# Performance work log

Measured on AMD Instinct MI355X. Metric: run time of the kernel, lower is better.

Reference implementation:

```python
import jax, jax.numpy as jnp
import numpy as np
from jax import lax

B, T, I, H, O = 4096, 512, 10, 32, 1

def setup_inputs() -> dict:
    key = jax.random.key(0)
    ks = jax.random.split(key, 7)
    s = 1.0 / np.sqrt(H)
    return {
        "x": jax.random.normal(ks[0], (B, T, I), dtype=jnp.float32),
        "W_ih": jax.random.uniform(ks[1], (4 * H, I), minval=-s, maxval=s, dtype=jnp.float32),
        "W_hh": jax.random.uniform(ks[2], (4 * H, H), minval=-s, maxval=s, dtype=jnp.float32),
        "b_ih": jax.random.uniform(ks[3], (4 * H,), minval=-s, maxval=s, dtype=jnp.float32),
        "b_hh": jax.random.uniform(ks[4], (4 * H,), minval=-s, maxval=s, dtype=jnp.float32),
        "W_dense": jax.random.uniform(ks[5], (O, H), minval=-s, maxval=s, dtype=jnp.float32),
        "b_dense": jax.random.uniform(ks[6], (O,), minval=-s, maxval=s, dtype=jnp.float32),
    }

def reference(x, W_ih, W_hh, b_ih, b_hh, W_dense, b_dense):
    # x: [B, T, I]; PyTorch LSTM gate order: i, f, g, o.
    b, t, _ = x.shape
    h = W_hh.shape[1]
    # Precompute input contribution for all timesteps: [T, B, 4H]
    gates_x = jnp.einsum('bti,gi->tbg', x, W_ih) + b_ih + b_hh

    def step(carry, gx):
        h_prev, c_prev = carry
        g = gx + h_prev @ W_hh.T  # [B, 4H]
        i_g = jax.nn.sigmoid(g[:, 0 * h:1 * h])
        f_g = jax.nn.sigmoid(g[:, 1 * h:2 * h])
        g_g = jnp.tanh(g[:, 2 * h:3 * h])
        o_g = jax.nn.sigmoid(g[:, 3 * h:4 * h])
        c = f_g * c_prev + i_g * g_g
        h_new = o_g * jnp.tanh(c)
        return (h_new, c), None

    init = (jnp.zeros((b, h), x.dtype), jnp.zeros((b, h), x.dtype))
    (h_last, _), _ = lax.scan(step, init, gates_x)
    # dropout in eval mode = identity
    return h_last @ W_dense.T + b_dense
```

## Files before the change

kernel.cpp:

```cpp
#include <hip/hip_runtime.h>


#define T_SZ 512
#define I_SZ 10
#define H_SZ 32

typedef _Float16 half8  __attribute__((ext_vector_type(8)));
typedef __fp16   fp16x2 __attribute__((ext_vector_type(2)));
typedef float    f32x4  __attribute__((ext_vector_type(4)));
typedef int      i32x4  __attribute__((ext_vector_type(4)));

union FH { i32x4 i; half8 h; };
static __device__ __forceinline__ half8 fragv(i32x4 v) { FH u; u.i = v; return u.h; }
static __device__ __forceinline__ half8 frag4(int a, int b, int c, int d) {
    FH u; u.i = (i32x4){a, b, c, d}; return u.h;
}

static __device__ __forceinline__ int pk16(float lo, float hi) {
    union { fp16x2 h; int i; } u;
    u.h = __builtin_amdgcn_cvt_pkrtz(lo, hi);
    return u.i;
}

#define MFMAH(A, B, C) __builtin_amdgcn_mfma_f32_16x16x32_f16((A), (B), (C), 0, 0, 0)

__global__ __launch_bounds__(64, 2)
void lstm_wave(const float* __restrict__ x, const float* __restrict__ W_ih,
               const float* __restrict__ W_hh, const float* __restrict__ b_ih,
               const float* __restrict__ b_hh, const float* __restrict__ W_dense,
               const float* __restrict__ b_dense, float* __restrict__ out)
{
    const int lane  = threadIdx.x;
    const int L     = lane & 15;
    const int Q     = lane >> 4;
    const int bbase = blockIdx.x * 2;

    const int bA   = L >> 3;
    const int bAct = Q >> 1;
    const int hidA = L + 16 * (Q & 1);

    int bhh[8][4];
    int bm[8][4];
    #pragma unroll
    for (int tau = 0; tau < 8; ++tau) {
        const int wr = 32 * (tau >> 1) + 16 * (tau & 1) + L;
        const float* ph = W_hh + wr * H_SZ + 8 * Q;
        #pragma unroll
        for (int d = 0; d < 4; ++d) {
            float2 v = *(const float2*)(ph + 2 * d);
            bhh[tau][d] = pk16(v.x, v.y);
        }
        if (Q == 0) {
            const float* pi = W_ih + wr * I_SZ;
            #pragma unroll
            for (int d = 0; d < 4; ++d) {
                float2 v = *(const float2*)(pi + 2 * d);
                bm[tau][d] = pk16(v.x, v.y);
            }
        } else if (Q == 1) {
            float2 v = *(const float2*)(W_ih + wr * I_SZ + 8);
            bm[tau][0] = pk16(v.x, v.y);
            #pragma unroll
            for (int d = 1; d < 4; ++d) {
                float2 w = *(const float2*)(W_hh + wr * H_SZ + 8 + 2 * d);
                bm[tau][d] = pk16(w.x, w.y);
            }
        } else {
            bm[tau][0] = bhh[tau][0]; bm[tau][1] = bhh[tau][1];
            bm[tau][2] = bhh[tau][2]; bm[tau][3] = bhh[tau][3];
        }
    }

    const float nL = -1.4426950f;
    const float m2 = -2.8853901f;
    const float mbi = nL * (b_ih[hidA]          + b_hh[hidA]);
    const float mbf = nL * (b_ih[32 + hidA]     + b_hh[32 + hidA]);
    const float mbg = m2 * (b_ih[64 + hidA]     + b_hh[64 + hidA]);
    const float mbo = nL * (b_ih[96 + hidA]     + b_hh[96 + hidA]);

    __shared__ __attribute__((aligned(16))) _Float16 hbuf[2][2][2][H_SZ];
    {
        int* zz = (int*)&hbuf[0][0][0][0];
        zz[lane] = 0;
        zz[lane + 64] = 0;
    }

    const float* xrow = x + (size_t)(bbase + bA) * (T_SZ * I_SZ);
    float2 xa0 = *(const float2*)(xrow + 0), xa1 = *(const float2*)(xrow + 2),
           xa2 = *(const float2*)(xrow + 4), xa3 = *(const float2*)(xrow + 6),
           xa4 = *(const float2*)(xrow + 8);
    float2 xb0 = *(const float2*)(xrow + I_SZ + 0), xb1 = *(const float2*)(xrow + I_SZ + 2),
           xb2 = *(const float2*)(xrow + I_SZ + 4), xb3 = *(const float2*)(xrow + I_SZ + 6),
           xb4 = *(const float2*)(xrow + I_SZ + 8);

    const f32x4 zerov = {0.f, 0.f, 0.f, 0.f};
    float cst = 0.0f;
    float hlast = 0.0f;
    const bool q0 = (Q == 0), q1 = (Q == 1);

    for (int t = 0; t < T_SZ; t += 2) {
        #pragma unroll
        for (int u = 0; u < 2; ++u) {
            const int rb = u, wb = u ^ 1;

            const _Float16* hp = &hbuf[rb][0][bA][8 * Q];
            const _Float16* lp = &hbuf[rb][1][bA][8 * Q];
            i32x4 hhi_ = *(const i32x4*)hp;
            i32x4 lo_  = *(const i32x4*)lp;

            float2 y0 = u ? xb0 : xa0, y1 = u ? xb1 : xa1, y2 = u ? xb2 : xa2,
                   y3 = u ? xb3 : xa3, y4 = u ? xb4 : xa4;
            int p0 = pk16(y0.x, y0.y), p1 = pk16(y1.x, y1.y), p2 = pk16(y2.x, y2.y),
                p3 = pk16(y3.x, y3.y), p4 = pk16(y4.x, y4.y);

            half8 mf = fragv((i32x4){ q0 ? p0 : (q1 ? p4 : lo_[0]),
                                      q0 ? p1 : lo_[1],
                                      q0 ? p2 : lo_[2],
                                      q0 ? p3 : lo_[3] });

            if (t + 2 + u < T_SZ) {
                const float* xr = xrow + (t + 2 + u) * I_SZ;
                if (u == 0) {
                    xa0 = *(const float2*)(xr + 0); xa1 = *(const float2*)(xr + 2);
                    xa2 = *(const float2*)(xr + 4); xa3 = *(const float2*)(xr + 6);
                    xa4 = *(const float2*)(xr + 8);
                } else {
                    xb0 = *(const float2*)(xr + 0); xb1 = *(const float2*)(xr + 2);
                    xb2 = *(const float2*)(xr + 4); xb3 = *(const float2*)(xr + 6);
                    xb4 = *(const float2*)(xr + 8);
                }
            }

            half8 hhi = fragv(hhi_);
            float v[8];
            #pragma unroll
            for (int tau = 0; tau < 8; ++tau) {
                f32x4 acc = MFMAH(mf, frag4(bm[tau][0], bm[tau][1], bm[tau][2], bm[tau][3]), zerov);
                acc = MFMAH(hhi, frag4(bhh[tau][0], bhh[tau][1], bhh[tau][2], bhh[tau][3]), acc);
                v[tau] = acc[0];
            }

            const bool qh = (Q & 1);
            float vi = qh ? v[1] : v[0];
            float vf = qh ? v[3] : v[2];
            float vg = qh ? v[5] : v[4];
            float vo = qh ? v[7] : v[6];
            float ig = __builtin_amdgcn_rcpf(1.0f + __builtin_amdgcn_exp2f(fmaf(nL, vi, mbi)));
            float fg = __builtin_amdgcn_rcpf(1.0f + __builtin_amdgcn_exp2f(fmaf(nL, vf, mbf)));
            float gr = __builtin_amdgcn_rcpf(1.0f + __builtin_amdgcn_exp2f(fmaf(m2, vg, mbg)));
            float gg = fmaf(2.0f, gr, -1.0f);
            float og = __builtin_amdgcn_rcpf(1.0f + __builtin_amdgcn_exp2f(fmaf(nL, vo, mbo)));
            cst = fmaf(fg, cst, ig * gg);
            float tr = __builtin_amdgcn_rcpf(1.0f + __builtin_amdgcn_exp2f(m2 * cst));
            float th = fmaf(2.0f, tr, -1.0f);
            float h  = og * th;
            hlast = h;

            _Float16 hh = (_Float16)h;
            _Float16 hl = (_Float16)(h - (float)hh);
            hbuf[wb][0][bAct][hidA] = hh;
            hbuf[wb][1][bAct][hidA] = hl;
        }
    }

    float v = hlast * W_dense[hidA];
    #pragma unroll
    for (int m = 16; m >= 1; m >>= 1)
        v += __shfl_xor(v, m);
    if (lane == 0)  out[bbase + 0] = v + b_dense[0];
    if (lane == 32) out[bbase + 1] = v + b_dense[0];
}

extern "C" void kernel_launch(void* const* d_in, const int* in_sizes, int n_in,
                              void* d_out, int out_size, void* d_ws, size_t ws_size,
                              hipStream_t stream) {
    const float* x       = (const float*)d_in[0];
    const float* W_ih    = (const float*)d_in[1];
    const float* W_hh    = (const float*)d_in[2];
    const float* b_ih    = (const float*)d_in[3];
    const float* b_hh    = (const float*)d_in[4];
    const float* W_dense = (const float*)d_in[5];
    const float* b_dense = (const float*)d_in[6];
    float* out = (float*)d_out;

    lstm_wave<<<dim3(2048), dim3(64), 0, stream>>>(
        x, W_ih, W_hh, b_ih, b_hh, W_dense, b_dense, out);
}
```

Baseline: 363.4 us.

## Pack four batch rows per wave, halving grid and doubling per-lane gate work

Each 64-lane wave now handles four batch sequences instead of two. Every lane computes two hidden units, one from each half of the MFMA output, and the grid is halved. The intent is to use the otherwise redundant MFMA rows and cut wave count, trading fewer waves for a longer per-step serial activation chain in each lane. There is a risk of lower latency hiding, since each wave has a longer per-step critical path and fewer waves run overall.

```diff
diff --git a/kernel.cpp b/kernel.cpp
--- a/kernel.cpp
+++ b/kernel.cpp
@@ -24,7 +24,7 @@
 
 #define MFMAH(A, B, C) __builtin_amdgcn_mfma_f32_16x16x32_f16((A), (B), (C), 0, 0, 0)
 
-__global__ __launch_bounds__(64, 2)
+__global__ __launch_bounds__(64, 1)
 void lstm_wave(const float* __restrict__ x, const float* __restrict__ W_ih,
                const float* __restrict__ W_hh, const float* __restrict__ b_ih,
                const float* __restrict__ b_hh, const float* __restrict__ W_dense,
@@ -33,11 +33,10 @@
     const int lane  = threadIdx.x;
     const int L     = lane & 15;
     const int Q     = lane >> 4;
-    const int bbase = blockIdx.x * 2;
+    const int bbase = blockIdx.x * 4;
 
-    const int bA   = L >> 3;
-    const int bAct = Q >> 1;
-    const int hidA = L + 16 * (Q & 1);
+    const int bA = L >> 2;
+    const int h0 = L, h1 = L + 16;
 
     int bhh[8][4];
     int bm[8][4];
@@ -73,16 +72,19 @@
 
     const float nL = -1.4426950f;
     const float m2 = -2.8853901f;
-    const float mbi = nL * (b_ih[hidA]          + b_hh[hidA]);
-    const float mbf = nL * (b_ih[32 + hidA]     + b_hh[32 + hidA]);
-    const float mbg = m2 * (b_ih[64 + hidA]     + b_hh[64 + hidA]);
-    const float mbo = nL * (b_ih[96 + hidA]     + b_hh[96 + hidA]);
+    const float mbi0 = nL * (b_ih[h0]      + b_hh[h0]);
+    const float mbf0 = nL * (b_ih[32 + h0] + b_hh[32 + h0]);
+    const float mbg0 = m2 * (b_ih[64 + h0] + b_hh[64 + h0]);
+    const float mbo0 = nL * (b_ih[96 + h0] + b_hh[96 + h0]);
+    const float mbi1 = nL * (b_ih[h1]      + b_hh[h1]);
+    const float mbf1 = nL * (b_ih[32 + h1] + b_hh[32 + h1]);
+    const float mbg1 = m2 * (b_ih[64 + h1] + b_hh[64 + h1]);
+    const float mbo1 = nL * (b_ih[96 + h1] + b_hh[96 + h1]);
 
-    __shared__ __attribute__((aligned(16))) _Float16 hbuf[2][2][2][H_SZ];
+    __shared__ __attribute__((aligned(16))) _Float16 hbuf[2][2][4][H_SZ];
     {
         int* zz = (int*)&hbuf[0][0][0][0];
-        zz[lane] = 0;
-        zz[lane + 64] = 0;
+        zz[lane] = 0; zz[lane + 64] = 0; zz[lane + 128] = 0; zz[lane + 192] = 0;
     }
 
     const float* xrow = x + (size_t)(bbase + bA) * (T_SZ * I_SZ);
@@ -94,8 +96,8 @@
            xb4 = *(const float2*)(xrow + I_SZ + 8);
 
     const f32x4 zerov = {0.f, 0.f, 0.f, 0.f};
-    float cst = 0.0f;
-    float hlast = 0.0f;
+    float cst0 = 0.0f, cst1 = 0.0f;
+    float h0last = 0.0f, h1last = 0.0f;
     const bool q0 = (Q == 0), q1 = (Q == 1);
 
     for (int t = 0; t < T_SZ; t += 2) {
@@ -140,35 +142,44 @@
                 v[tau] = acc[0];
             }
 
-            const bool qh = (Q & 1);
-            float vi = qh ? v[1] : v[0];
-            float vf = qh ? v[3] : v[2];
-            float vg = qh ? v[5] : v[4];
-            float vo = qh ? v[7] : v[6];
-            float ig = __builtin_amdgcn_rcpf(1.0f + __builtin_amdgcn_exp2f(fmaf(nL, vi, mbi)));
-            float fg = __builtin_amdgcn_rcpf(1.0f + __builtin_amdgcn_exp2f(fmaf(nL, vf, mbf)));
-            float gr = __builtin_amdgcn_rcpf(1.0f + __builtin_amdgcn_exp2f(fmaf(m2, vg, mbg)));
-            float gg = fmaf(2.0f, gr, -1.0f);
-            float og = __builtin_amdgcn_rcpf(1.0f + __builtin_amdgcn_exp2f(fmaf(nL, vo, mbo)));
-            cst = fmaf(fg, cst, ig * gg);
-            float tr = __builtin_amdgcn_rcpf(1.0f + __builtin_amdgcn_exp2f(m2 * cst));
-            float th = fmaf(2.0f, tr, -1.0f);
-            float h  = og * th;
-            hlast = h;
+            float ig0 = __builtin_amdgcn_rcpf(1.0f + __builtin_amdgcn_exp2f(fmaf(nL, v[0], mbi0)));
+            float fg0 = __builtin_amdgcn_rcpf(1.0f + __builtin_amdgcn_exp2f(fmaf(nL, v[2], mbf0)));
+            float gr0 = __builtin_amdgcn_rcpf(1.0f + __builtin_amdgcn_exp2f(fmaf(m2, v[4], mbg0)));
+            float gg0 = fmaf(2.0f, gr0, -1.0f);
+            float og0 = __builtin_amdgcn_rcpf(1.0f + __builtin_amdgcn_exp2f(fmaf(nL, v[6], mbo0)));
+            cst0 = fmaf(fg0, cst0, ig0 * gg0);
+            float tr0 = __builtin_amdgcn_rcpf(1.0f + __builtin_amdgcn_exp2f(m2 * cst0));
+            float th0 = fmaf(2.0f, tr0, -1.0f);
+            float hv0 = og0 * th0;
+            h0last = hv0;
 
-            _Float16 hh = (_Float16)h;
-            _Float16 hl = (_Float16)(h - (float)hh);
-            hbuf[wb][0][bAct][hidA] = hh;
-            hbuf[wb][1][bAct][hidA] = hl;
+            float ig1 = __builtin_amdgcn_rcpf(1.0f + __builtin_amdgcn_exp2f(fmaf(nL, v[1], mbi1)));
+            float fg1 = __builtin_amdgcn_rcpf(1.0f + __builtin_amdgcn_exp2f(fmaf(nL, v[3], mbf1)));
+            float gr1 = __builtin_amdgcn_rcpf(1.0f + __builtin_amdgcn_exp2f(fmaf(m2, v[5], mbg1)));
+            float gg1 = fmaf(2.0f, gr1, -1.0f);
+            float og1 = __builtin_amdgcn_rcpf(1.0f + __builtin_amdgcn_exp2f(fmaf(nL, v[7], mbo1)));
+            cst1 = fmaf(fg1, cst1, ig1 * gg1);
+            float tr1 = __builtin_amdgcn_rcpf(1.0f + __builtin_amdgcn_exp2f(m2 * cst1));
+            float th1 = fmaf(2.0f, tr1, -1.0f);
+            float hv1 = og1 * th1;
+            h1last = hv1;
+
+            _Float16 a0h = (_Float16)hv0;
+            _Float16 a0l = (_Float16)(hv0 - (float)a0h);
+            _Float16 a1h = (_Float16)hv1;
+            _Float16 a1l = (_Float16)(hv1 - (float)a1h);
+            hbuf[wb][0][Q][h0] = a0h;
+            hbuf[wb][0][Q][h1] = a1h;
+            hbuf[wb][1][Q][h0] = a0l;
+            hbuf[wb][1][Q][h1] = a1l;
         }
     }
 
-    float v = hlast * W_dense[hidA];
+    float v = h0last * W_dense[h0] + h1last * W_dense[h1];
     #pragma unroll
-    for (int m = 16; m >= 1; m >>= 1)
+    for (int m = 8; m >= 1; m >>= 1)
         v += __shfl_xor(v, m);
-    if (lane == 0)  out[bbase + 0] = v + b_dense[0];
-    if (lane == 32) out[bbase + 1] = v + b_dense[0];
+    if (L == 0) out[bbase + Q] = v + b_dense[0];
 }
 
 extern "C" void kernel_launch(void* const* d_in, const int* in_sizes, int n_in,
@@ -183,6 +194,6 @@
     const float* b_dense = (const float*)d_in[6];
     float* out = (float*)d_out;
 
-    lstm_wave<<<dim3(2048), dim3(64), 0, stream>>>(
+    lstm_wave<<<dim3(1024), dim3(64), 0, stream>>>(
         x, W_ih, W_hh, b_ih, b_hh, W_dense, b_dense, out);
 }
```

After: 368.0 us. No clear change (+1.3%).

## Interleave two independent batch-pair recurrences per wave to hide MFMA latency

Applied to the files above, without the earlier changes.

Each 64-lane wave now advances two independent pairs of batch rows (four sequences) together, running the MFMA chains and gate math for both in the same timestep. The two dependency chains can overlap, filling MFMA and transcendental latency that a single serial recurrence leaves idle. The grid is halved to 1024 waves and launch bounds relaxed to one wave per EU, which raises register pressure and cuts the number of concurrent waves.

```diff
diff --git a/kernel.cpp b/kernel.cpp
--- a/kernel.cpp
+++ b/kernel.cpp
@@ -24,7 +24,7 @@
 
 #define MFMAH(A, B, C) __builtin_amdgcn_mfma_f32_16x16x32_f16((A), (B), (C), 0, 0, 0)
 
-__global__ __launch_bounds__(64, 2)
+__global__ __launch_bounds__(64, 1)
 void lstm_wave(const float* __restrict__ x, const float* __restrict__ W_ih,
                const float* __restrict__ W_hh, const float* __restrict__ b_ih,
                const float* __restrict__ b_hh, const float* __restrict__ W_dense,
@@ -33,9 +33,9 @@
     const int lane  = threadIdx.x;
     const int L     = lane & 15;
     const int Q     = lane >> 4;
-    const int bbase = blockIdx.x * 2;
-
-    const int bA   = L >> 3;
+    const int bbase = blockIdx.x * 4;
+
+    const int bAg  = L >> 3;
     const int bAct = Q >> 1;
     const int hidA = L + 16 * (Q & 1);
 
@@ -73,102 +73,154 @@
 
     const float nL = -1.4426950f;
     const float m2 = -2.8853901f;
-    const float mbi = nL * (b_ih[hidA]          + b_hh[hidA]);
-    const float mbf = nL * (b_ih[32 + hidA]     + b_hh[32 + hidA]);
-    const float mbg = m2 * (b_ih[64 + hidA]     + b_hh[64 + hidA]);
-    const float mbo = nL * (b_ih[96 + hidA]     + b_hh[96 + hidA]);
-
-    __shared__ __attribute__((aligned(16))) _Float16 hbuf[2][2][2][H_SZ];
+    const float mbi = nL * (b_ih[hidA]      + b_hh[hidA]);
+    const float mbf = nL * (b_ih[32 + hidA] + b_hh[32 + hidA]);
+    const float mbg = m2 * (b_ih[64 + hidA] + b_hh[64 + hidA]);
+    const float mbo = nL * (b_ih[96 + hidA] + b_hh[96 + hidA]);
+
+    __shared__ __attribute__((aligned(16))) _Float16 hbuf[2][2][4][H_SZ];
     {
         int* zz = (int*)&hbuf[0][0][0][0];
-        zz[lane] = 0;
-        zz[lane + 64] = 0;
-    }
-
-    const float* xrow = x + (size_t)(bbase + bA) * (T_SZ * I_SZ);
-    float2 xa0 = *(const float2*)(xrow + 0), xa1 = *(const float2*)(xrow + 2),
-           xa2 = *(const float2*)(xrow + 4), xa3 = *(const float2*)(xrow + 6),
-           xa4 = *(const float2*)(xrow + 8);
-    float2 xb0 = *(const float2*)(xrow + I_SZ + 0), xb1 = *(const float2*)(xrow + I_SZ + 2),
-           xb2 = *(const float2*)(xrow + I_SZ + 4), xb3 = *(const float2*)(xrow + I_SZ + 6),
-           xb4 = *(const float2*)(xrow + I_SZ + 8);
+        zz[lane] = 0; zz[lane + 64] = 0; zz[lane + 128] = 0; zz[lane + 192] = 0;
+    }
+
+    const float* xrowX = x + (size_t)(bbase + bAg)     * (T_SZ * I_SZ);
+    const float* xrowY = x + (size_t)(bbase + 2 + bAg) * (T_SZ * I_SZ);
+    float2 xA0 = *(const float2*)(xrowX + 0), xA1 = *(const float2*)(xrowX + 2),
+           xA2 = *(const float2*)(xrowX + 4), xA3 = *(const float2*)(xrowX + 6),
+           xA4 = *(const float2*)(xrowX + 8);
+    float2 xB0 = *(const float2*)(xrowX + I_SZ + 0), xB1 = *(const float2*)(xrowX + I_SZ + 2),
+           xB2 = *(const float2*)(xrowX + I_SZ + 4), xB3 = *(const float2*)(xrowX + I_SZ + 6),
+           xB4 = *(const float2*)(xrowX + I_SZ + 8);
+    float2 yA0 = *(const float2*)(xrowY + 0), yA1 = *(const float2*)(xrowY + 2),
+           yA2 = *(const float2*)(xrowY + 4), yA3 = *(const float2*)(xrowY + 6),
+           yA4 = *(const float2*)(xrowY + 8);
+    float2 yB0 = *(const float2*)(xrowY + I_SZ + 0), yB1 = *(const float2*)(xrowY + I_SZ + 2),
+           yB2 = *(const float2*)(xrowY + I_SZ + 4), yB3 = *(const float2*)(xrowY + I_SZ + 6),
+           yB4 = *(const float2*)(xrowY + I_SZ + 8);
 
     const f32x4 zerov = {0.f, 0.f, 0.f, 0.f};
-    float cst = 0.0f;
-    float hlast = 0.0f;
+    float cstX = 0.0f, cstY = 0.0f;
+    float hXlast = 0.0f, hYlast = 0.0f;
     const bool q0 = (Q == 0), q1 = (Q == 1);
+    const bool qh = (Q & 1);
 
     for (int t = 0; t < T_SZ; t += 2) {
         #pragma unroll
         for (int u = 0; u < 2; ++u) {
             const int rb = u, wb = u ^ 1;
 
-            const _Float16* hp = &hbuf[rb][0][bA][8 * Q];
-            const _Float16* lp = &hbuf[rb][1][bA][8 * Q];
-            i32x4 hhi_ = *(const i32x4*)hp;
-            i32x4 lo_  = *(const i32x4*)lp;
-
-            float2 y0 = u ? xb0 : xa0, y1 = u ? xb1 : xa1, y2 = u ? xb2 : xa2,
-                   y3 = u ? xb3 : xa3, y4 = u ? xb4 : xa4;
-            int p0 = pk16(y0.x, y0.y), p1 = pk16(y1.x, y1.y), p2 = pk16(y2.x, y2.y),
-                p3 = pk16(y3.x, y3.y), p4 = pk16(y4.x, y4.y);
-
-            half8 mf = fragv((i32x4){ q0 ? p0 : (q1 ? p4 : lo_[0]),
-                                      q0 ? p1 : lo_[1],
-                                      q0 ? p2 : lo_[2],
-                                      q0 ? p3 : lo_[3] });
+            i32x4 hhiX_ = *(const i32x4*)&hbuf[rb][0][bAg][8 * Q];
+            i32x4 loX_  = *(const i32x4*)&hbuf[rb][1][bAg][8 * Q];
+            float2 u0 = u ? xB0 : xA0, u1 = u ? xB1 : xA1, u2 = u ? xB2 : xA2,
+                   u3 = u ? xB3 : xA3, u4 = u ? xB4 : xA4;
+            int pX0 = pk16(u0.x, u0.y), pX1 = pk16(u1.x, u1.y), pX2 = pk16(u2.x, u2.y),
+                pX3 = pk16(u3.x, u3.y), pX4 = pk16(u4.x, u4.y);
+            half8 mfX = fragv((i32x4){ q0 ? pX0 : (q1 ? pX4 : loX_[0]),
+                                       q0 ? pX1 : loX_[1],
+                                       q0 ? pX2 : loX_[2],
+                                       q0 ? pX3 : loX_[3] });
+            half8 hhiX = fragv(hhiX_);
+            float vX[8];
+            #pragma unroll
+            for (int tau = 0; tau < 8; ++tau) {
+                f32x4 acc = MFMAH(mfX, frag4(bm[tau][0], bm[tau][1], bm[tau][2], bm[tau][3]), zerov);
+                acc = MFMAH(hhiX, frag4(bhh[tau][0], bhh[tau][1], bhh[tau][2], bhh[tau][3]), acc);
+                vX[tau] = acc[0];
+            }
+
+            i32x4 hhiY_ = *(const i32x4*)&hbuf[rb][0][2 + bAg][8 * Q];
+            i32x4 loY_  = *(const i32x4*)&hbuf[rb][1][2 + bAg][8 * Q];
+            float2 w0 = u ? yB0 : yA0, w1 = u ? yB1 : yA1, w2 = u ? yB2 : yA2,
+                   w3 = u ? yB3 : yA3, w4 = u ? yB4 : yA4;
+            int pY0 = pk16(w0.x, w0.y), pY1 = pk16(w1.x, w1.y), pY2 = pk16(w2.x, w2.y),
+                pY3 = pk16(w3.x, w3.y), pY4 = pk16(w4.x, w4.y);
+            half8 mfY = fragv((i32x4){ q0 ? pY0 : (q1 ? pY4 : loY_[0]),
+                                       q0 ? pY1 : loY_[1],
+                                       q0 ? pY2 : loY_[2],
+                                       q0 ? pY3 : loY_[3] });
+            half8 hhiY = fragv(hhiY_);
+            float vY[8];
+            #pragma unroll
+            for (int tau = 0; tau < 8; ++tau) {
+                f32x4 acc = MFMAH(mfY, frag4(bm[tau][0], bm[tau][1], bm[tau][2], bm[tau][3]), zerov);
+                acc = MFMAH(hhiY, frag4(bhh[tau][0], bhh[tau][1], bhh[tau][2], bhh[tau][3]), acc);
+                vY[tau] = acc[0];
+            }
 
             if (t + 2 + u < T_SZ) {
-                const float* xr = xrow + (t + 2 + u) * I_SZ;
+                const float* xrX = xrowX + (t + 2 + u) * I_SZ;
+                const float* xrY = xrowY + (t + 2 + u) * I_SZ;
                 if (u == 0) {
-                    xa0 = *(const float2*)(xr + 0); xa1 = *(const float2*)(xr + 2);
-                    xa2 = *(const float2*)(xr + 4); xa3 = *(const float2*)(xr + 6);
-                    xa4 = *(const float2*)(xr + 8);
+                    xA0 = *(const float2*)(xrX + 0); xA1 = *(const float2*)(xrX + 2);
+                    xA2 = *(const float2*)(xrX + 4); xA3 = *(const float2*)(xrX + 6);
+                    xA4 = *(const float2*)(xrX + 8);
+                    yA0 = *(const float2*)(xrY + 0); yA1 = *(const float2*)(xrY + 2);
+                    yA2 = *(const float2*)(xrY + 4); yA3 = *(const float2*)(xrY + 6);
+                    yA4 = *(const float2*)(xrY + 8);
                 } else {
-                    xb0 = *(const float2*)(xr + 0); xb1 = *(const float2*)(xr + 2);
-                    xb2 = *(const float2*)(xr + 4); xb3 = *(const float2*)(xr + 6);
-                    xb4 = *(const float2*)(xr + 8);
+                    xB0 = *(const float2*)(xrX + 0); xB1 = *(const float2*)(xrX + 2);
+                    xB2 = *(const float2*)(xrX + 4); xB3 = *(const float2*)(xrX + 6);
+                    xB4 = *(const float2*)(xrX + 8);
+                    yB0 = *(const float2*)(xrY + 0); yB1 = *(const float2*)(xrY + 2);
+                    yB2 = *(const float2*)(xrY + 4); yB3 = *(const float2*)(xrY + 6);
+                    yB4 = *(const float2*)(xrY + 8);
                 }
             }
 
-            half8 hhi = fragv(hhi_);
-            float v[8];
-            #pragma unroll
-            for (int tau = 0; tau < 8; ++tau) {
-                f32x4 acc = MFMAH(mf, frag4(bm[tau][0], bm[tau][1], bm[tau][2], bm[tau][3]), zerov);
-                acc = MFMAH(hhi, frag4(bhh[tau][0], bhh[tau][1], bhh[tau][2], bhh[tau][3]), acc);
-                v[tau] = acc[0];
-            }
-
-            const bool qh = (Q & 1);
-            float vi = qh ? v[1] : v[0];
-            float vf = qh ? v[3] : v[2];
-            float vg = qh ? v[5] : v[4];
-            float vo = qh ? v[7] : v[6];
-            float ig = __builtin_amdgcn_rcpf(1.0f + __builtin_amdgcn_exp2f(fmaf(nL, vi, mbi)));
-            float fg = __builtin_amdgcn_rcpf(1.0f + __builtin_amdgcn_exp2f(fmaf(nL, vf, mbf)));
-            float gr = __builtin_amdgcn_rcpf(1.0f + __builtin_amdgcn_exp2f(fmaf(m2, vg, mbg)));
-            float gg = fmaf(2.0f, gr, -1.0f);
-            float og = __builtin_amdgcn_rcpf(1.0f + __builtin_amdgcn_exp2f(fmaf(nL, vo, mbo)));
-            cst = fmaf(fg, cst, ig * gg);
-            float tr = __builtin_amdgcn_rcpf(1.0f + __builtin_amdgcn_exp2f(m2 * cst));
-            float th = fmaf(2.0f, tr, -1.0f);
-            float h  = og * th;
-            hlast = h;
-
-            _Float16 hh = (_Float16)h;
-            _Float16 hl = (_Float16)(h - (float)hh);
-            hbuf[wb][0][bAct][hidA] = hh;
-            hbuf[wb][1][bAct][hidA] = hl;
+            {
+                float vi = qh ? vX[1] : vX[0];
+                float vf = qh ? vX[3] : vX[2];
+                float vg = qh ? vX[5] : vX[4];
+                float vo = qh ? vX[7] : vX[6];
+                float ig = __builtin_amdgcn_rcpf(1.0f + __builtin_amdgcn_exp2f(fmaf(nL, vi, mbi)));
+                float fg = __builtin_amdgcn_rcpf(1.0f + __builtin_amdgcn_exp2f(fmaf(nL, vf, mbf)));
+                float gr = __builtin_amdgcn_rcpf(1.0f + __builtin_amdgcn_exp2f(fmaf(m2, vg, mbg)));
+                float gg = fmaf(2.0f, gr, -1.0f);
+                float og = __builtin_amdgcn_rcpf(1.0f + __builtin_amdgcn_exp2f(fmaf(nL, vo, mbo)));
+                cstX = fmaf(fg, cstX, ig * gg);
+                float tr = __builtin_amdgcn_rcpf(1.0f + __builtin_amdgcn_exp2f(m2 * cstX));
+                float th = fmaf(2.0f, tr, -1.0f);
+                float h  = og * th;
+                hXlast = h;
+                _Float16 hh = (_Float16)h;
+                _Float16 hl = (_Float16)(h - (float)hh);
+                hbuf[wb][0][bAct][hidA] = hh;
+                hbuf[wb][1][bAct][hidA] = hl;
+            }
+
+            {
+                float vi = qh ? vY[1] : vY[0];
+                float vf = qh ? vY[3] : vY[2];
+                float vg = qh ? vY[5] : vY[4];
+                float vo = qh ? vY[7] : vY[6];
+                float ig = __builtin_amdgcn_rcpf(1.0f + __builtin_amdgcn_exp2f(fmaf(nL, vi, mbi)));
+                float fg = __builtin_amdgcn_rcpf(1.0f + __builtin_amdgcn_exp2f(fmaf(nL, vf, mbf)));
+                float gr = __builtin_amdgcn_rcpf(1.0f + __builtin_amdgcn_exp2f(fmaf(m2, vg, mbg)));
+                float gg = fmaf(2.0f, gr, -1.0f);
+                float og = __builtin_amdgcn_rcpf(1.0f + __builtin_amdgcn_exp2f(fmaf(nL, vo, mbo)));
+                cstY = fmaf(fg, cstY, ig * gg);
+                float tr = __builtin_amdgcn_rcpf(1.0f + __builtin_amdgcn_exp2f(m2 * cstY));
+                float th = fmaf(2.0f, tr, -1.0f);
+                float h  = og * th;
+                hYlast = h;
+                _Float16 hh = (_Float16)h;
+                _Float16 hl = (_Float16)(h - (float)hh);
+                hbuf[wb][0][2 + bAct][hidA] = hh;
+                hbuf[wb][1][2 + bAct][hidA] = hl;
+            }
         }
     }
 
-    float v = hlast * W_dense[hidA];
+    float vx = hXlast * W_dense[hidA];
+    float vy = hYlast * W_dense[hidA];
     #pragma unroll
-    for (int m = 16; m >= 1; m >>= 1)
-        v += __shfl_xor(v, m);
-    if (lane == 0)  out[bbase + 0] = v + b_dense[0];
-    if (lane == 32) out[bbase + 1] = v + b_dense[0];
+    for (int m = 16; m >= 1; m >>= 1) {
+        vx += __shfl_xor(vx, m);
+        vy += __shfl_xor(vy, m);
+    }
+    if (lane == 0)  { out[bbase + 0] = vx + b_dense[0]; out[bbase + 2] = vy + b_dense[0]; }
+    if (lane == 32) { out[bbase + 1] = vx + b_dense[0]; out[bbase + 3] = vy + b_dense[0]; }
 }
 
 extern "C" void kernel_launch(void* const* d_in, const int* in_sizes, int n_in,
@@ -183,6 +235,6 @@
     const float* b_dense = (const float*)d_in[6];
     float* out = (float*)d_out;
 
-    lstm_wave<<<dim3(2048), dim3(64), 0, stream>>>(
+    lstm_wave<<<dim3(1024), dim3(64), 0, stream>>>(
         x, W_ih, W_hh, b_ih, b_hh, W_dense, b_dense, out);
 }
```

Measured after the change: 412.0 us. +13.4%, slower.

## Interleave gate exps with MFMAs, merge reciprocals, stagger waves with priority hints

Applied to the files above, without the earlier changes.

Reorders the per-step MFMA chain so each gate's exp2 is issued as soon as its pair of MFMAs finishes, overlapping transcendental work with the remaining matrix ops. It folds the sigmoid and tanh algebra so the input-gate times cell-gate product and the output-gate times tanh(c) product each need a single reciprocal instead of two, shortening the serial dependency chain per timestep. It also raises wave priority around the MFMA block and sleeps half the blocks briefly at start to desynchronise waves sharing a CU. The merged reciprocals multiply two (1+e) terms, which can overflow for large negative pre-activations, and the stagger and priority hints may have no effect.

```diff
diff --git a/kernel.cpp b/kernel.cpp
--- a/kernel.cpp
+++ b/kernel.cpp
@@ -23,6 +23,8 @@
 }
 
 #define MFMAH(A, B, C) __builtin_amdgcn_mfma_f32_16x16x32_f16((A), (B), (C), 0, 0, 0)
+#define EXP2(x) __builtin_amdgcn_exp2f(x)
+#define RCP(x)  __builtin_amdgcn_rcpf(x)
 
 __global__ __launch_bounds__(64, 2)
 void lstm_wave(const float* __restrict__ x, const float* __restrict__ W_ih,
@@ -73,10 +75,10 @@
 
     const float nL = -1.4426950f;
     const float m2 = -2.8853901f;
-    const float mbi = nL * (b_ih[hidA]          + b_hh[hidA]);
-    const float mbf = nL * (b_ih[32 + hidA]     + b_hh[32 + hidA]);
-    const float mbg = m2 * (b_ih[64 + hidA]     + b_hh[64 + hidA]);
-    const float mbo = nL * (b_ih[96 + hidA]     + b_hh[96 + hidA]);
+    const float mbi = nL * (b_ih[hidA]      + b_hh[hidA]);
+    const float mbf = nL * (b_ih[32 + hidA] + b_hh[32 + hidA]);
+    const float mbg = m2 * (b_ih[64 + hidA] + b_hh[64 + hidA]);
+    const float mbo = nL * (b_ih[96 + hidA] + b_hh[96 + hidA]);
 
     __shared__ __attribute__((aligned(16))) _Float16 hbuf[2][2][2][H_SZ];
     {
@@ -97,16 +99,18 @@
     float cst = 0.0f;
     float hlast = 0.0f;
     const bool q0 = (Q == 0), q1 = (Q == 1);
+    const bool qh = (Q & 1);
+
+    if ((blockIdx.x >> 10) & 1)
+        __builtin_amdgcn_s_sleep(8);
 
     for (int t = 0; t < T_SZ; t += 2) {
         #pragma unroll
         for (int u = 0; u < 2; ++u) {
             const int rb = u, wb = u ^ 1;
 
-            const _Float16* hp = &hbuf[rb][0][bA][8 * Q];
-            const _Float16* lp = &hbuf[rb][1][bA][8 * Q];
-            i32x4 hhi_ = *(const i32x4*)hp;
-            i32x4 lo_  = *(const i32x4*)lp;
+            i32x4 hhi_ = *(const i32x4*)&hbuf[rb][0][bA][8 * Q];
+            i32x4 lo_  = *(const i32x4*)&hbuf[rb][1][bA][8 * Q];
 
             float2 y0 = u ? xb0 : xa0, y1 = u ? xb1 : xa1, y2 = u ? xb2 : xa2,
                    y3 = u ? xb3 : xa3, y4 = u ? xb4 : xa4;
@@ -117,6 +121,33 @@
                                       q0 ? p1 : lo_[1],
                                       q0 ? p2 : lo_[2],
                                       q0 ? p3 : lo_[3] });
+            half8 hhi = fragv(hhi_);
+
+            __builtin_amdgcn_s_setprio(1);
+            f32x4 a0 = MFMAH(mf,  frag4(bm[0][0],  bm[0][1],  bm[0][2],  bm[0][3]),  zerov);
+            a0       = MFMAH(hhi, frag4(bhh[0][0], bhh[0][1], bhh[0][2], bhh[0][3]), a0);
+            f32x4 a1 = MFMAH(mf,  frag4(bm[1][0],  bm[1][1],  bm[1][2],  bm[1][3]),  zerov);
+            a1       = MFMAH(hhi, frag4(bhh[1][0], bhh[1][1], bhh[1][2], bhh[1][3]), a1);
+            float eA = EXP2(fmaf(nL, qh ? a1[0] : a0[0], mbi));
+
+            f32x4 a2 = MFMAH(mf,  frag4(bm[2][0],  bm[2][1],  bm[2][2],  bm[2][3]),  zerov);
+            a2       = MFMAH(hhi, frag4(bhh[2][0], bhh[2][1], bhh[2][2], bhh[2][3]), a2);
+            f32x4 a3 = MFMAH(mf,  frag4(bm[3][0],  bm[3][1],  bm[3][2],  bm[3][3]),  zerov);
+            a3       = MFMAH(hhi, frag4(bhh[3][0], bhh[3][1], bhh[3][2], bhh[3][3]), a3);
+            float eF = EXP2(fmaf(nL, qh ? a3[0] : a2[0], mbf));
+
+            f32x4 a4 = MFMAH(mf,  frag4(bm[4][0],  bm[4][1],  bm[4][2],  bm[4][3]),  zerov);
+            a4       = MFMAH(hhi, frag4(bhh[4][0], bhh[4][1], bhh[4][2], bhh[4][3]), a4);
+            f32x4 a5 = MFMAH(mf,  frag4(bm[5][0],  bm[5][1],  bm[5][2],  bm[5][3]),  zerov);
+            a5       = MFMAH(hhi, frag4(bhh[5][0], bhh[5][1], bhh[5][2], bhh[5][3]), a5);
+            float eG = EXP2(fmaf(m2, qh ? a5[0] : a4[0], mbg));
+
+            f32x4 a6 = MFMAH(mf,  frag4(bm[6][0],  bm[6][1],  bm[6][2],  bm[6][3]),  zerov);
+            a6       = MFMAH(hhi, frag4(bhh[6][0], bhh[6][1], bhh[6][2], bhh[6][3]), a6);
+            f32x4 a7 = MFMAH(mf,  frag4(bm[7][0],  bm[7][1],  bm[7][2],  bm[7][3]),  zerov);
+            a7       = MFMAH(hhi, frag4(bhh[7][0], bhh[7][1], bhh[7][2], bhh[7][3]), a7);
+            __builtin_amdgcn_s_setprio(0);
+            float eO = EXP2(fmaf(nL, qh ? a7[0] : a6[0], mbo));
 
             if (t + 2 + u < T_SZ) {
                 const float* xr = xrow + (t + 2 + u) * I_SZ;
@@ -131,33 +162,15 @@
                 }
             }
 
-            half8 hhi = fragv(hhi_);
-            float v[8];
-            #pragma unroll
-            for (int tau = 0; tau < 8; ++tau) {
-                f32x4 acc = MFMAH(mf, frag4(bm[tau][0], bm[tau][1], bm[tau][2], bm[tau][3]), zerov);
-                acc = MFMAH(hhi, frag4(bhh[tau][0], bhh[tau][1], bhh[tau][2], bhh[tau][3]), acc);
-                v[tau] = acc[0];
-            }
-
-            const bool qh = (Q & 1);
-            float vi = qh ? v[1] : v[0];
-            float vf = qh ? v[3] : v[2];
-            float vg = qh ? v[5] : v[4];
-            float vo = qh ? v[7] : v[6];
-            float ig = __builtin_amdgcn_rcpf(1.0f + __builtin_amdgcn_exp2f(fmaf(nL, vi, mbi)));
-            float fg = __builtin_amdgcn_rcpf(1.0f + __builtin_amdgcn_exp2f(fmaf(nL, vf, mbf)));
-            float gr = __builtin_amdgcn_rcpf(1.0f + __builtin_amdgcn_exp2f(fmaf(m2, vg, mbg)));
-            float gg = fmaf(2.0f, gr, -1.0f);
-            float og = __builtin_amdgcn_rcpf(1.0f + __builtin_amdgcn_exp2f(fmaf(nL, vo, mbo)));
-            cst = fmaf(fg, cst, ig * gg);
-            float tr = __builtin_amdgcn_rcpf(1.0f + __builtin_amdgcn_exp2f(m2 * cst));
-            float th = fmaf(2.0f, tr, -1.0f);
-            float h  = og * th;
-            hlast = h;
-
-            _Float16 hh = (_Float16)h;
-            _Float16 hl = (_Float16)(h - (float)hh);
+            float fg  = RCP(1.0f + eF);
+            float igg = (1.0f - eG) * RCP((1.0f + eA) * (1.0f + eG));
+            cst = fmaf(fg, cst, igg);
+            float eD = EXP2(m2 * cst);
+            float hv = (1.0f - eD) * RCP((1.0f + eO) * (1.0f + eD));
+            hlast = hv;
+
+            _Float16 hh = (_Float16)hv;
+            _Float16 hl = (_Float16)(hv - (float)hh);
             hbuf[wb][0][bAct][hidA] = hh;
             hbuf[wb][1][bAct][hidA] = hl;
         }
```

Result: faster. 333.3 us (-8.3%).
